# Kernel optimization log

Hardware: AMD Instinct MI355X
Metric: run time of the kernel (lower is better)

The kernel has to match this reference:

```python
import jax, jax.numpy as jnp
import numpy as np

B, C, E = 4, 2048, 1024
H, D = 16, 64


def setup_inputs() -> dict:
    key = jax.random.key(0)
    kx, kq, kk, kv, ko = jax.random.split(key, 5)
    s = 0.02
    return {
        "x": jax.random.normal(kx, (B, C, E), dtype=jnp.float32),
        "W_q": jax.random.normal(kq, (E, H * D), dtype=jnp.float32) * s,
        "W_k": jax.random.normal(kk, (E, H * D), dtype=jnp.float32) * s,
        "W_v": jax.random.normal(kv, (E, H * D), dtype=jnp.float32) * s,
        "W_o": jax.random.normal(ko, (H * D, E), dtype=jnp.float32) * s,
    }


def reference(x, W_q, W_k, W_v, W_o):
    b, c, e = x.shape
    # projections -> [B, H, C, D]
    def split_heads(t):
        return t.reshape(b, c, H, D).transpose(0, 2, 1, 3)
    Q = split_heads(x @ W_q)
    K = split_heads(x @ W_k)
    V = split_heads(x @ W_v)
    scale = 1.0 / jnp.sqrt(jnp.asarray(D, dtype=x.dtype))
    scores = jnp.einsum("bhqd,bhkd->bhqk", Q, K) * scale  # [B,H,C,C]
    causal = jnp.tril(jnp.ones((c, c), dtype=bool))
    scores = jnp.where(causal, scores, jnp.asarray(-jnp.inf, dtype=scores.dtype))
    weights = jax.nn.softmax(scores, axis=-1)
    hidden = jnp.einsum("bhqk,bhkd->bhqd", weights, V)  # [B,H,C,D]
    hidden = hidden.transpose(0, 2, 1, 3).reshape(b, c, H * D)
    return hidden @ W_o
```

## Files before the change

kernel.cpp:

```cpp
#include <hip/hip_runtime.h>

typedef __bf16 bf16;
typedef __attribute__((ext_vector_type(8))) __bf16 bf16x8;
typedef __attribute__((ext_vector_type(4))) __bf16 bf16x4;
typedef __attribute__((ext_vector_type(4))) float f32x4;
typedef __attribute__((ext_vector_type(16))) float f32x16;

#define B_ 4
#define C_ 2048
#define E_ 1024
#define H_ 16
#define D_ 64

__device__ __forceinline__ void gload16(const void* g, void* l) {
  __builtin_amdgcn_global_load_lds(
      (const __attribute__((address_space(1))) void*)g,
      (__attribute__((address_space(3))) void*)l, 16, 0, 0);
}

__device__ __forceinline__ unsigned cvtpk(float lo, float hi) {
  unsigned r;
  asm("v_cvt_pk_bf16_f32 %0, %1, %2" : "=v"(r) : "v"(lo), "v"(hi));
  return r;
}
__device__ __forceinline__ void pswap(unsigned& a, unsigned& b) {
  asm volatile("v_permlane32_swap_b32 %0, %1" : "+v"(a), "+v"(b));
}
__device__ __forceinline__ bf16x8 mkfrag(unsigned d0, unsigned d1, unsigned d2,
                                         unsigned d3) {
  union {
    unsigned u[4];
    bf16x8 v;
  } x;
  x.u[0] = d0;
  x.u[1] = d1;
  x.u[2] = d2;
  x.u[3] = d3;
  return x.v;
}

__global__ __launch_bounds__(256) void prep(const float* __restrict__ x,
                                            const float* __restrict__ Wq,
                                            const float* __restrict__ Wk,
                                            const float* __restrict__ Wv,
                                            const float* __restrict__ Wo,
                                            bf16* __restrict__ xb,
                                            bf16* __restrict__ WT) {
  if (blockIdx.z < 4) {
    const float* W = blockIdx.z == 0 ? Wq : blockIdx.z == 1 ? Wk
                   : blockIdx.z == 2 ? Wv : Wo;
    bf16* dst = WT + (size_t)blockIdx.z * 1024 * 1024;
    __shared__ bf16 t[64][65];
    const int tx = threadIdx.x & 63, ty = threadIdx.x >> 6;
    const int r0 = blockIdx.y * 64, c0 = blockIdx.x * 64;
#pragma unroll
    for (int r = ty; r < 64; r += 4)
      t[tx][r] = (__bf16)W[(size_t)(r0 + r) * 1024 + c0 + tx];
    __syncthreads();
#pragma unroll
    for (int r = ty; r < 64; r += 4)
      dst[(size_t)(c0 + r) * 1024 + r0 + tx] = t[r][tx];
  } else {
    const size_t chunk =
        ((size_t)(blockIdx.z - 4) * 256 + blockIdx.y * 16 + blockIdx.x);
    const size_t i = chunk * 256 + threadIdx.x;
    const float4* p = (const float4*)(x + i * 8);
    float4 a = p[0], b = p[1];
    bf16x8 v = {(__bf16)a.x, (__bf16)a.y, (__bf16)a.z, (__bf16)a.w,
                (__bf16)b.x, (__bf16)b.y, (__bf16)b.z, (__bf16)b.w};
    *(bf16x8*)(xb + i * 8) = v;
  }
}

template <int MODE>
__global__ __launch_bounds__(256, 2) void gemm_bt(const bf16* __restrict__ A,
                                                  const bf16* __restrict__ WTall,
                                                  bf16* __restrict__ Qo,
                                                  bf16* __restrict__ Ko,
                                                  bf16* __restrict__ Vto,
                                                  float* __restrict__ Fo) {
  constexpr int BK = 64;
  constexpr int NT = 1024 / BK;
  const int tid = threadIdx.x;
  const int wave = tid >> 6, lane = tid & 63;
  const int cl = lane & 15, g = lane >> 4;
  const int wr = wave >> 1, wc = wave & 1;
  const int brow = blockIdx.x * 128;
  const int bcol = blockIdx.y * 128;
  const bf16* Bt =
      (MODE == 0) ? (WTall + (size_t)blockIdx.z * 1024 * 1024) : WTall;

  __shared__ __align__(16) bf16 ldsA[2][128 * BK];
  __shared__ __align__(16) bf16 ldsB[2][128 * BK];

  f32x4 acc[4][4] = {};

  auto STAGE = [&](int kt, int buf) {
#pragma unroll
    for (int it = 0; it < 4; ++it) {
      const int chunk = it * 256 + tid;
      const int row = chunk >> 3, slot = chunk & 7;
      const int se = (slot ^ (row & 7)) * 8;
      const int ldsoff = (it * 256 + wave * 64) * 16;
      gload16(A + (size_t)(brow + row) * 1024 + kt + se,
              (char*)&ldsA[buf][0] + ldsoff);
      gload16(Bt + (size_t)(bcol + row) * 1024 + kt + se,
              (char*)&ldsB[buf][0] + ldsoff);
    }
  };

  STAGE(0, 0);
  STAGE(BK, 1);
  asm volatile("s_waitcnt vmcnt(8)" ::: "memory");
  __builtin_amdgcn_s_barrier();

  for (int t = 0; t < NT; ++t) {
    const int buf = t & 1;
    bf16x8 af0[4], bf0[4], af1[4], bf1[4];
#pragma unroll
    for (int i = 0; i < 4; ++i) {
      const int sl = (g ^ (cl & 7)) * 8;
      af0[i] = *(const bf16x8*)&ldsA[buf][(wr * 64 + i * 16 + cl) * BK + sl];
      bf0[i] = *(const bf16x8*)&ldsB[buf][(wc * 64 + i * 16 + cl) * BK + sl];
    }
    __builtin_amdgcn_sched_barrier(0);
#pragma unroll
    for (int i = 0; i < 4; ++i) {
      const int sl = ((4 + g) ^ (cl & 7)) * 8;
      af1[i] = *(const bf16x8*)&ldsA[buf][(wr * 64 + i * 16 + cl) * BK + sl];
      bf1[i] = *(const bf16x8*)&ldsB[buf][(wc * 64 + i * 16 + cl) * BK + sl];
    }
    asm volatile("s_waitcnt lgkmcnt(8)" ::: "memory");
    __builtin_amdgcn_sched_barrier(0);
#pragma unroll
    for (int i = 0; i < 4; ++i)
#pragma unroll
      for (int j = 0; j < 4; ++j)
        acc[i][j] = __builtin_amdgcn_mfma_f32_16x16x32_bf16(af0[i], bf0[j],
                                                            acc[i][j], 0, 0, 0);
    asm volatile("s_waitcnt lgkmcnt(0)" ::: "memory");
    __builtin_amdgcn_sched_barrier(0);
#pragma unroll
    for (int i = 0; i < 4; ++i)
#pragma unroll
      for (int j = 0; j < 4; ++j)
        acc[i][j] = __builtin_amdgcn_mfma_f32_16x16x32_bf16(af1[i], bf1[j],
                                                            acc[i][j], 0, 0, 0);
    __builtin_amdgcn_s_barrier();
    if (t + 2 < NT) {
      STAGE((t + 2) * BK, buf);
      asm volatile("s_waitcnt vmcnt(8)" ::: "memory");
    } else {
      asm volatile("s_waitcnt vmcnt(0)" ::: "memory");
    }
    __builtin_amdgcn_s_barrier();
  }

  if constexpr (MODE == 0) {
    if (blockIdx.z == 2) {
      bf16* tb = &ldsA[0][0];
#pragma unroll
      for (int i = 0; i < 4; ++i) {
#pragma unroll
        for (int j = 0; j < 4; ++j) {
          const int gc_l = wc * 64 + j * 16 + cl;
          const int gr0 = wr * 64 + i * 16 + g * 4;
          bf16x4 pk = {(__bf16)acc[i][j][0], (__bf16)acc[i][j][1],
                       (__bf16)acc[i][j][2], (__bf16)acc[i][j][3]};
          *(bf16x4*)&tb[gc_l * 128 + (gr0 ^ ((gc_l & 7) << 4))] = pk;
        }
      }
      __syncthreads();
      const int b = brow >> 11;
      const int cbase = brow & 2047;
#pragma unroll
      for (int p = 0; p < 8; ++p) {
        const int rowl = p * 16 + (tid >> 4);
        const int col0 = (tid & 15) * 8;
        bf16x8 vv = *(const bf16x8*)&tb[rowl * 128 + (col0 ^ ((rowl & 7) << 4))];
        const int gc = bcol + rowl;
        const int hh = gc >> 6, dd = gc & 63;
        *(bf16x8*)&Vto[(((size_t)b * H_ + hh) * D_ + dd) * C_ + cbase + col0] =
            vv;
      }
    } else {
      bf16* dst = blockIdx.z == 0 ? Qo : Ko;
      const float presc = (blockIdx.z == 0) ? 0.18033688011112042f : 1.0f;
#pragma unroll
      for (int i = 0; i < 4; ++i) {
#pragma unroll
        for (int j = 0; j < 4; ++j) {
#pragma unroll
          for (int r = 0; r < 4; ++r) {
            const int gr = brow + wr * 64 + i * 16 + g * 4 + r;
            const int gc = bcol + wc * 64 + j * 16 + cl;
            const float v = acc[i][j][r] * presc;
            const int b = gr >> 11, c = gr & 2047;
            const int h = gc >> 6, d = gc & 63;
            dst[(((size_t)b * H_ + h) * C_ + c) * D_ + d] = (__bf16)v;
          }
        }
      }
    }
  } else {
#pragma unroll
    for (int i = 0; i < 4; ++i)
#pragma unroll
      for (int j = 0; j < 4; ++j)
#pragma unroll
        for (int r = 0; r < 4; ++r) {
          const int gr = brow + wr * 64 + i * 16 + g * 4 + r;
          const int gc = bcol + wc * 64 + j * 16 + cl;
          Fo[(size_t)gr * 1024 + gc] = acc[i][j][r];
        }
  }
}

__device__ __forceinline__ void sm_fixed(f32x16& s0, f32x16& s1, f32x4& l4,
                                         int th0, bool domask, int hi,
                                         bf16x8& pf0, bf16x8& pf1,
                                         bf16x8& pf2, bf16x8& pf3) {
  if (domask) {
#pragma unroll
    for (int r = 0; r < 16; ++r) {
      const int crow = (r & 3) + 8 * (r >> 2) + 4 * hi;
      if (crow > th0) s0[r] = -1e30f;
      if (crow + 32 > th0) s1[r] = -1e30f;
    }
  }
#pragma unroll
  for (int r = 0; r < 16; ++r) {
    s0[r] = __builtin_amdgcn_exp2f(s0[r]);
    s1[r] = __builtin_amdgcn_exp2f(s1[r]);
  }
#pragma unroll
  for (int r = 0; r < 16; ++r) l4[r & 3] += s0[r] + s1[r];
  unsigned a0 = cvtpk(s0[0], s0[1]), a1 = cvtpk(s0[2], s0[3]);
  unsigned b0 = cvtpk(s0[4], s0[5]), b1 = cvtpk(s0[6], s0[7]);
  unsigned c0 = cvtpk(s0[8], s0[9]), c1 = cvtpk(s0[10], s0[11]);
  unsigned d0 = cvtpk(s0[12], s0[13]), d1 = cvtpk(s0[14], s0[15]);
  unsigned e0 = cvtpk(s1[0], s1[1]), e1 = cvtpk(s1[2], s1[3]);
  unsigned f0 = cvtpk(s1[4], s1[5]), f1 = cvtpk(s1[6], s1[7]);
  unsigned g0 = cvtpk(s1[8], s1[9]), g1 = cvtpk(s1[10], s1[11]);
  unsigned h0 = cvtpk(s1[12], s1[13]), h1 = cvtpk(s1[14], s1[15]);
  pswap(a0, b0);
  pswap(a1, b1);
  pswap(c0, d0);
  pswap(c1, d1);
  pswap(e0, f0);
  pswap(e1, f1);
  pswap(g0, h0);
  pswap(g1, h1);
  pf0 = mkfrag(a0, a1, b0, b1);
  pf1 = mkfrag(c0, c1, d0, d1);
  pf2 = mkfrag(e0, e1, f0, f1);
  pf3 = mkfrag(g0, g1, h0, h1);
}

__global__ __launch_bounds__(256, 2) void attn(const bf16* __restrict__ Qg,
                                               const bf16* __restrict__ Kg,
                                               const bf16* __restrict__ Vt,
                                               bf16* __restrict__ Hid) {
  const int tid = threadIdx.x, wave = tid >> 6, lane = tid & 63;
  const int l31 = lane & 31, hi = lane >> 5, l7 = lane & 7;
  const int qa = blockIdx.x, qb = 15 - (int)blockIdx.x;
  const int h = blockIdx.y, b = blockIdx.z;
  const size_t bh = (size_t)b * H_ + h;

  __shared__ __align__(16) bf16 ldsK[2 * 128 * 64];
  __shared__ __align__(16) bf16 ldsV[2 * 64 * 128];

  const bf16* Kb = Kg + bh * C_ * D_;
  const bf16* Vb = Vt + bh * (size_t)D_ * C_;

  const int qrowA = qa * 128 + wave * 32;
  const int qrowB = qb * 128 + wave * 32;

  bf16x8 qfA[4], qfB[4];
  {
    const bf16* qra = Qg + (bh * C_ + qrowA + l31) * D_;
    const bf16* qrb = Qg + (bh * C_ + qrowB + l31) * D_;
#pragma unroll
    for (int ds = 0; ds < 4; ++ds) {
      qfA[ds] = *(const bf16x8*)(qra + ds * 16 + 8 * hi);
      qfB[ds] = *(const bf16x8*)(qrb + ds * 16 + 8 * hi);
    }
  }

  f32x4 l4A = {}, l4B = {};
  f32x16 oA0 = {}, oA1 = {}, oB0 = {}, oB1 = {};

  auto STAGE = [&](int kt, int buf) {
#pragma unroll
    for (int w = 0; w < 4; ++w) {
      const int chunk = w * 256 + tid;
      {
        const int row = chunk >> 3, slot = chunk & 7;
        const int se = (slot ^ (row & 7)) * 8;
        gload16(Kb + ((size_t)kt * 128 + row) * D_ + se,
                (char*)ldsK + buf * 16384 + (w * 256 + wave * 64) * 16);
      }
      {
        const int row = chunk >> 4, slot = chunk & 15;
        const int se = (slot ^ (row & 7)) * 8;
        gload16(Vb + (size_t)row * C_ + kt * 128 + se,
                (char*)ldsV + buf * 16384 + (w * 256 + wave * 64) * 16);
      }
    }
  };

  const int nkv = qb + 1;
  STAGE(0, 0);

  for (int kt = 0; kt < nkv; ++kt) {
    const int cur = kt & 1;
    const bf16* kb = ldsK + cur * 8192;
    const bf16* vb = ldsV + cur * 8192;
    if (kt + 1 < nkv) {
      STAGE(kt + 1, cur ^ 1);
      asm volatile("s_waitcnt vmcnt(8)" ::: "memory");
    } else {
      asm volatile("s_waitcnt vmcnt(0)" ::: "memory");
    }
    __builtin_amdgcn_s_barrier();
    __builtin_amdgcn_sched_barrier(0);

#pragma unroll
    for (int hh = 0; hh < 2; ++hh) {
      const int key0 = kt * 128 + hh * 64;
      const bool actA = (key0 <= qrowA + 31);
      const bool actB = (key0 <= qrowB + 31);
      if (!actA && !actB) continue;

      f32x16 sA0 = {}, sA1 = {}, sB0 = {}, sB1 = {};
      __builtin_amdgcn_s_setprio(1);
#pragma unroll
      for (int ds = 0; ds < 4; ++ds) {
        const int r0 = hh * 64 + l31, r1 = hh * 64 + 32 + l31;
        bf16x8 kf0 = *(const bf16x8*)&kb[r0 * 64 + (((2 * ds + hi) ^ (r0 & 7)) * 8)];
        bf16x8 kf1 = *(const bf16x8*)&kb[r1 * 64 + (((2 * ds + hi) ^ (r1 & 7)) * 8)];
        if (actA) {
          sA0 = __builtin_amdgcn_mfma_f32_32x32x16_bf16(kf0, qfA[ds], sA0, 0, 0, 0);
          sA1 = __builtin_amdgcn_mfma_f32_32x32x16_bf16(kf1, qfA[ds], sA1, 0, 0, 0);
        }
        if (actB) {
          sB0 = __builtin_amdgcn_mfma_f32_32x32x16_bf16(kf0, qfB[ds], sB0, 0, 0, 0);
          sB1 = __builtin_amdgcn_mfma_f32_32x32x16_bf16(kf1, qfB[ds], sB1, 0, 0, 0);
        }
      }
      __builtin_amdgcn_s_setprio(0);

      bf16x8 vf0[4], vf1[4];
#pragma unroll
      for (int ks = 0; ks < 4; ++ks) {
        const int gs = hh * 8 + 2 * ks + hi;
        vf0[ks] = *(const bf16x8*)&vb[l31 * 128 + ((gs ^ (l31 & 7)) * 8)];
        vf1[ks] = *(const bf16x8*)&vb[(32 + l31) * 128 + ((gs ^ ((32 + l31) & 7)) * 8)];
      }

      if (actA) {
        bf16x8 p0, p1, p2, p3;
        sm_fixed(sA0, sA1, l4A, qrowA + l31 - key0, key0 + 63 > qrowA, hi,
                 p0, p1, p2, p3);
        __builtin_amdgcn_s_setprio(1);
        oA0 = __builtin_amdgcn_mfma_f32_32x32x16_bf16(vf0[0], p0, oA0, 0, 0, 0);
        oA1 = __builtin_amdgcn_mfma_f32_32x32x16_bf16(vf1[0], p0, oA1, 0, 0, 0);
        oA0 = __builtin_amdgcn_mfma_f32_32x32x16_bf16(vf0[1], p1, oA0, 0, 0, 0);
        oA1 = __builtin_amdgcn_mfma_f32_32x32x16_bf16(vf1[1], p1, oA1, 0, 0, 0);
        oA0 = __builtin_amdgcn_mfma_f32_32x32x16_bf16(vf0[2], p2, oA0, 0, 0, 0);
        oA1 = __builtin_amdgcn_mfma_f32_32x32x16_bf16(vf1[2], p2, oA1, 0, 0, 0);
        oA0 = __builtin_amdgcn_mfma_f32_32x32x16_bf16(vf0[3], p3, oA0, 0, 0, 0);
        oA1 = __builtin_amdgcn_mfma_f32_32x32x16_bf16(vf1[3], p3, oA1, 0, 0, 0);
        __builtin_amdgcn_s_setprio(0);
      }
      if (actB) {
        bf16x8 p0, p1, p2, p3;
        sm_fixed(sB0, sB1, l4B, qrowB + l31 - key0, key0 + 63 > qrowB, hi,
                 p0, p1, p2, p3);
        __builtin_amdgcn_s_setprio(1);
        oB0 = __builtin_amdgcn_mfma_f32_32x32x16_bf16(vf0[0], p0, oB0, 0, 0, 0);
        oB1 = __builtin_amdgcn_mfma_f32_32x32x16_bf16(vf1[0], p0, oB1, 0, 0, 0);
        oB0 = __builtin_amdgcn_mfma_f32_32x32x16_bf16(vf0[1], p1, oB0, 0, 0, 0);
        oB1 = __builtin_amdgcn_mfma_f32_32x32x16_bf16(vf1[1], p1, oB1, 0, 0, 0);
        oB0 = __builtin_amdgcn_mfma_f32_32x32x16_bf16(vf0[2], p2, oB0, 0, 0, 0);
        oB1 = __builtin_amdgcn_mfma_f32_32x32x16_bf16(vf1[2], p2, oB1, 0, 0, 0);
        oB0 = __builtin_amdgcn_mfma_f32_32x32x16_bf16(vf0[3], p3, oB0, 0, 0, 0);
        oB1 = __builtin_amdgcn_mfma_f32_32x32x16_bf16(vf1[3], p3, oB1, 0, 0, 0);
        __builtin_amdgcn_s_setprio(0);
      }
    }
    __builtin_amdgcn_s_barrier();
  }

#pragma unroll
  for (int st = 0; st < 2; ++st) {
    const f32x4 l4 = st ? l4B : l4A;
    float l = (l4[0] + l4[1]) + (l4[2] + l4[3]);
    l += __shfl_xor(l, 32, 64);
    const float inv = 1.0f / l;
    const int qrow = st ? qrowB : qrowA;
    const size_t row = (size_t)b * C_ + qrow + l31;
#pragma unroll
    for (int dt = 0; dt < 2; ++dt) {
      const f32x16& oo = st ? (dt ? oB1 : oB0) : (dt ? oA1 : oA0);
#pragma unroll
      for (int q4 = 0; q4 < 4; ++q4) {
        bf16x4 pk = {(__bf16)(oo[4 * q4 + 0] * inv),
                     (__bf16)(oo[4 * q4 + 1] * inv),
                     (__bf16)(oo[4 * q4 + 2] * inv),
                     (__bf16)(oo[4 * q4 + 3] * inv)};
        const int d = dt * 32 + 8 * q4 + 4 * hi;
        *(bf16x4*)&Hid[row * (H_ * D_) + h * 64 + d] = pk;
      }
    }
  }
}

extern "C" void kernel_launch(void* const* d_in, const int* in_sizes, int n_in,
                              void* d_out, int out_size, void* d_ws,
                              size_t ws_size, hipStream_t stream) {
  const float* x = (const float*)d_in[0];
  const float* Wq = (const float*)d_in[1];
  const float* Wk = (const float*)d_in[2];
  const float* Wv = (const float*)d_in[3];
  const float* Wo = (const float*)d_in[4];

  char* ws = (char*)d_ws;
  bf16* xb = (bf16*)ws;
  bf16* WT = (bf16*)(ws + (16ull << 20));
  bf16* Qb = (bf16*)(ws + (24ull << 20));
  bf16* Kb = (bf16*)(ws + (40ull << 20));
  bf16* Vtb = (bf16*)(ws + (56ull << 20));
  bf16* Hid = (bf16*)(ws + (72ull << 20));

  prep<<<dim3(16, 16, 20), 256, 0, stream>>>(x, Wq, Wk, Wv, Wo, xb, WT);
  gemm_bt<0><<<dim3(64, 8, 3), 256, 0, stream>>>(xb, WT, Qb, Kb, Vtb, nullptr);
  attn<<<dim3(8, H_, B_), 256, 0, stream>>>(Qb, Kb, Vtb, Hid);
  gemm_bt<1><<<dim3(64, 8, 1), 256, 0, stream>>>(
      Hid, WT + 3ull * 1024 * 1024, nullptr, nullptr, nullptr, (float*)d_out);
}
```

Measured before the change: 153.7 us.

## Load K and V fragments directly from global memory instead of LDS staging

Removes the double-buffered LDS staging of K and V tiles (async global-to-LDS loads, waitcnt, and block barriers). Each wave now reads its K and V MFMA fragments straight from global memory. This drops shared-memory use and the per-tile barriers, but every wave re-fetches the same K/V data independently, which leaves reuse to the caches and loses the prefetch overlap of the next tile.

```diff
diff --git a/kernel.cpp b/kernel.cpp
--- a/kernel.cpp
+++ b/kernel.cpp
@@ -262,13 +262,10 @@
                                                const bf16* __restrict__ Vt,
                                                bf16* __restrict__ Hid) {
   const int tid = threadIdx.x, wave = tid >> 6, lane = tid & 63;
-  const int l31 = lane & 31, hi = lane >> 5, l7 = lane & 7;
+  const int l31 = lane & 31, hi = lane >> 5;
   const int qa = blockIdx.x, qb = 15 - (int)blockIdx.x;
   const int h = blockIdx.y, b = blockIdx.z;
   const size_t bh = (size_t)b * H_ + h;
-
-  __shared__ __align__(16) bf16 ldsK[2 * 128 * 64];
-  __shared__ __align__(16) bf16 ldsV[2 * 64 * 128];
 
   const bf16* Kb = Kg + bh * C_ * D_;
   const bf16* Vb = Vt + bh * (size_t)D_ * C_;
@@ -290,41 +287,9 @@
   f32x4 l4A = {}, l4B = {};
   f32x16 oA0 = {}, oA1 = {}, oB0 = {}, oB1 = {};
 
-  auto STAGE = [&](int kt, int buf) {
-#pragma unroll
-    for (int w = 0; w < 4; ++w) {
-      const int chunk = w * 256 + tid;
-      {
-        const int row = chunk >> 3, slot = chunk & 7;
-        const int se = (slot ^ (row & 7)) * 8;
-        gload16(Kb + ((size_t)kt * 128 + row) * D_ + se,
-                (char*)ldsK + buf * 16384 + (w * 256 + wave * 64) * 16);
-      }
-      {
-        const int row = chunk >> 4, slot = chunk & 15;
-        const int se = (slot ^ (row & 7)) * 8;
-        gload16(Vb + (size_t)row * C_ + kt * 128 + se,
-                (char*)ldsV + buf * 16384 + (w * 256 + wave * 64) * 16);
-      }
-    }
-  };
-
   const int nkv = qb + 1;
-  STAGE(0, 0);
 
   for (int kt = 0; kt < nkv; ++kt) {
-    const int cur = kt & 1;
-    const bf16* kb = ldsK + cur * 8192;
-    const bf16* vb = ldsV + cur * 8192;
-    if (kt + 1 < nkv) {
-      STAGE(kt + 1, cur ^ 1);
-      asm volatile("s_waitcnt vmcnt(8)" ::: "memory");
-    } else {
-      asm volatile("s_waitcnt vmcnt(0)" ::: "memory");
-    }
-    __builtin_amdgcn_s_barrier();
-    __builtin_amdgcn_sched_barrier(0);
-
 #pragma unroll
     for (int hh = 0; hh < 2; ++hh) {
       const int key0 = kt * 128 + hh * 64;
@@ -332,13 +297,14 @@
       const bool actB = (key0 <= qrowB + 31);
       if (!actA && !actB) continue;
 
+      const bf16* Krow = Kb + (size_t)key0 * D_;
       f32x16 sA0 = {}, sA1 = {}, sB0 = {}, sB1 = {};
       __builtin_amdgcn_s_setprio(1);
 #pragma unroll
       for (int ds = 0; ds < 4; ++ds) {
-        const int r0 = hh * 64 + l31, r1 = hh * 64 + 32 + l31;
-        bf16x8 kf0 = *(const bf16x8*)&kb[r0 * 64 + (((2 * ds + hi) ^ (r0 & 7)) * 8)];
-        bf16x8 kf1 = *(const bf16x8*)&kb[r1 * 64 + (((2 * ds + hi) ^ (r1 & 7)) * 8)];
+        bf16x8 kf0 = *(const bf16x8*)&Krow[(size_t)l31 * D_ + (2 * ds + hi) * 8];
+        bf16x8 kf1 =
+            *(const bf16x8*)&Krow[(size_t)(32 + l31) * D_ + (2 * ds + hi) * 8];
         if (actA) {
           sA0 = __builtin_amdgcn_mfma_f32_32x32x16_bf16(kf0, qfA[ds], sA0, 0, 0, 0);
           sA1 = __builtin_amdgcn_mfma_f32_32x32x16_bf16(kf1, qfA[ds], sA1, 0, 0, 0);
@@ -353,9 +319,9 @@
       bf16x8 vf0[4], vf1[4];
 #pragma unroll
       for (int ks = 0; ks < 4; ++ks) {
-        const int gs = hh * 8 + 2 * ks + hi;
-        vf0[ks] = *(const bf16x8*)&vb[l31 * 128 + ((gs ^ (l31 & 7)) * 8)];
-        vf1[ks] = *(const bf16x8*)&vb[(32 + l31) * 128 + ((gs ^ ((32 + l31) & 7)) * 8)];
+        const int col = kt * 128 + (hh * 8 + 2 * ks + hi) * 8;
+        vf0[ks] = *(const bf16x8*)&Vb[(size_t)l31 * C_ + col];
+        vf1[ks] = *(const bf16x8*)&Vb[(size_t)(32 + l31) * C_ + col];
       }
 
       if (actA) {
@@ -389,7 +355,6 @@
         __builtin_amdgcn_s_setprio(0);
       }
     }
-    __builtin_amdgcn_s_barrier();
   }
 
 #pragma unroll
```

Result: slower. 213.3 us (+38.8%).
